# Kernel optimization log

Hardware: AMD Instinct MI355X
Metric: run time of the kernel (lower is better)

The kernel has to match this reference:

```python
import jax, jax.numpy as jnp
import numpy as np

BN_EPS = 1e-5


def _conv1x1(x, w, b=None):
    # x: [B,C,H,W], w: [O,C] (1x1 conv kernel squeezed)
    y = jnp.einsum('bchw,oc->bohw', x, w)
    if b is not None:
        y = y + b[None, :, None, None]
    return y


def _maxpool2(x):
    B, C, H, W = x.shape
    return x.reshape(B, C, H // 2, 2, W // 2, 2).max(axis=(3, 5))


def setup_inputs() -> dict:
    key = jax.random.key(0)
    ks = jax.random.split(key, 14)
    B, C, H, W = 8, 128, 64, 64
    IC = C // 2  # inter_channels
    s = 0.05
    f32 = jnp.float32
    return {
        'x': jax.random.normal(ks[0], (B, C, H, W), f32),
        'w1': jax.random.normal(ks[1], (IC, C), f32) * s,
        'b1': jax.random.normal(ks[2], (IC,), f32) * s,
        'w3': jax.random.normal(ks[3], (IC, C), f32) * s,
        'b3': jax.random.normal(ks[4], (IC,), f32) * s,
        'w4': jax.random.normal(ks[5], (IC, C), f32) * s,
        'b4': jax.random.normal(ks[6], (IC,), f32) * s,
        'w5': jax.random.normal(ks[7], (2 * IC,), f32) * s,  # conv5_pr, no bias
        'w2': jax.random.normal(ks[8], (C, IC), f32) * s,  # zero-init in torch; randomized for a non-trivial baseline
        'b2': jax.random.normal(ks[9], (C,), f32) * s,
        'bn_gamma': 1.0 + jax.random.normal(ks[10], (C,), f32) * 0.1,
        'bn_beta': jax.random.normal(ks[11], (C,), f32) * 0.1,
        'bn_mean': jax.random.normal(ks[12], (C,), f32) * 0.1,
        'bn_var': jax.random.uniform(ks[13], (C,), f32, 0.5, 1.5),
    }


def reference(x, w1, b1, w3, b3, w4, b4, w5, w2, b2, bn_gamma, bn_beta, bn_mean, bn_var):
    B, C, H, W = x.shape
    IC = C // 2
    N = H * W            # query positions
    # value branch: conv1 -> maxpool -> [B, M, IC]
    xg = _maxpool2(_conv1x1(x, w1, b1)).reshape(B, IC, -1)  # [B, IC, M]
    M = xg.shape[-1]
    xg = xg.transpose(0, 2, 1)  # [B, M, IC]
    # affinity: relu(w5 . cat(xt_i, xp_j)) is separable -> avoid [B,2IC,N,M] blowup
    xt = _conv1x1(x, w3, b3).reshape(B, IC, N)              # [B, IC, N]
    xp = _maxpool2(_conv1x1(x, w4, b4)).reshape(B, IC, M)   # [B, IC, M]
    wt, wp = w5[:IC], w5[IC:]
    logits = jnp.einsum('c,bcn->bn', wt, xt)[:, :, None] + \
             jnp.einsum('c,bcm->bm', wp, xp)[:, None, :]    # [B, N, M]
    feats = jax.nn.relu(logits) / M
    # aggregate
    y = jnp.einsum('bnm,bmi->bni', feats, xg)               # [B, N, IC]
    y = y.transpose(0, 2, 1).reshape(B, IC, H, W)
    # conv2 + batchnorm (eval mode, running stats)
    y = _conv1x1(y, w2, b2)
    inv = jax.lax.rsqrt(bn_var + BN_EPS)
    y = (y - bn_mean[None, :, None, None]) * (bn_gamma * inv)[None, :, None, None] + bn_beta[None, :, None, None]
    return y + x
```

## Files before the change

kernel.cpp:

```cpp
#include <hip/hip_runtime.h>

typedef unsigned int u32;
typedef unsigned short u16;

#define Cn 128
#define ICn 64
#define Nn 4096
#define Mn 1024

typedef __attribute__((ext_vector_type(8))) short s8v;
typedef __attribute__((ext_vector_type(4))) float f4v;

union U8 { uint4 u; s8v v; };

__device__ __forceinline__ float asf(u32 u){ union{u32 i; float f;} v; v.i = u; return v.f; }
__device__ __forceinline__ float bf2f(u16 u){ return asf(((u32)u) << 16); }
__device__ __forceinline__ u32 pk2(float lo, float hi){
    u32 r;
    asm("v_cvt_pk_bf16_f32 %0, %1, %2" : "=v"(r) : "v"(lo), "v"(hi));
    return r;
}
__device__ __forceinline__ u16 f2bf(float f){ return (u16)pk2(f, f); }

__global__ __launch_bounds__(256) void k_conv(
    const float* __restrict__ x,
    const float* __restrict__ w1, const float* __restrict__ b1,
    const float* __restrict__ w3, const float* __restrict__ b3,
    const float* __restrict__ w4, const float* __restrict__ b4,
    const float* __restrict__ w5,
    float* __restrict__ t_o, float* __restrict__ p_o, u16* __restrict__ xg_o)
{
    const int tile = blockIdx.x;
    const int r  = tile >> 1;
    const int wb = tile & 1;
    const int b  = blockIdx.y;
    const int tid = threadIdx.x;

    __shared__ __align__(16) u16 smem[35080];
    u16* xsT = smem;
    u16* w1t = smem + 8704;
    u16* w4t = smem + 17408;
    float* u3s = (float*)&smem[26112];
    float* ph0 = (float*)&smem[26372];
    float* ph1 = (float*)&smem[30724];

    #pragma unroll
    for (int it = 0; it < 4; ++it) {
        int f = tid + 256 * it;
        int cp = f >> 4, rem = f & 15;
        int rl = rem >> 3, wq = rem & 7;
        const float* src = x + ((size_t)(b * Cn + 2 * cp)) * Nn + (2 * r + rl) * 64 + 32 * wb + 4 * wq;
        float4 v0 = *(const float4*)src;
        float4 v1 = *(const float4*)(src + Nn);
        int lp0 = rl * 32 + 4 * wq;
        int cS = (2 * cp) ^ (wq << 3);
        *(u32*)&xsT[(lp0 + 0) * 136 + cS] = pk2(v0.x, v1.x);
        *(u32*)&xsT[(lp0 + 1) * 136 + cS] = pk2(v0.y, v1.y);
        *(u32*)&xsT[(lp0 + 2) * 136 + cS] = pk2(v0.z, v1.z);
        *(u32*)&xsT[(lp0 + 3) * 136 + cS] = pk2(v0.w, v1.w);
    }
    #pragma unroll
    for (int it = 0; it < 4; ++it) {
        int f = tid + 256 * it;
        int ic = f >> 4, cq = f & 15;
        const float4* s1 = (const float4*)&w1[f * 8];
        const float4* s4 = (const float4*)&w4[f * 8];
        float4 a0 = s1[0], a1v = s1[1];
        float4 d0 = s4[0], d1v = s4[1];
        uint4 A, D;
        A.x = pk2(a0.x, a0.y); A.y = pk2(a0.z, a0.w); A.z = pk2(a1v.x, a1v.y); A.w = pk2(a1v.z, a1v.w);
        D.x = pk2(d0.x, d0.y); D.y = pk2(d0.z, d0.w); D.z = pk2(d1v.x, d1v.y); D.w = pk2(d1v.z, d1v.w);
        *(uint4*)&w1t[ic * 136 + 8 * cq] = A;
        *(uint4*)&w4t[ic * 136 + 8 * cq] = D;
    }
    if (tid < 128) {
        float s0 = 0.f, s1 = 0.f;
        #pragma unroll 8
        for (int ic = 0; ic < 64; ic += 2) {
            s0 += w5[ic]     * w3[ic * Cn + tid];
            s1 += w5[ic + 1] * w3[(ic + 1) * Cn + tid];
        }
        u3s[tid] = s0 + s1;
    } else if (tid == 128) {
        float s = 0.f;
        #pragma unroll 16
        for (int ic = 0; ic < 64; ++ic) s += w5[ic] * b3[ic];
        u3s[128] = s;
    }
    __syncthreads();

    const int lane = tid & 63;
    const int wv   = tid >> 6;
    const int col  = lane & 15;
    const int quad = lane >> 4;

    f4v acc1[4] = {}, acc4[4] = {};
    const u16* xrow = &xsT[(16 * wv + col) * 136];
    const int xsw = (((16 * wv + col) >> 2) & 7) << 3;
    #pragma unroll
    for (int kb = 0; kb < 4; ++kb) {
        s8v bx = *(const s8v*)&xrow[(kb * 32 + quad * 8) ^ xsw];
        #pragma unroll
        for (int icb = 0; icb < 4; ++icb) {
            s8v a1 = *(const s8v*)&w1t[(icb * 16 + col) * 136 + kb * 32 + quad * 8];
            s8v a4 = *(const s8v*)&w4t[(icb * 16 + col) * 136 + kb * 32 + quad * 8];
            acc1[icb] = __builtin_amdgcn_mfma_f32_16x16x32_bf16(a1, bx, acc1[icb], 0, 0, 0);
            acc4[icb] = __builtin_amdgcn_mfma_f32_16x16x32_bf16(a4, bx, acc4[icb], 0, 0, 0);
        }
    }

    const int lp = 16 * wv + col;
    const int rl = lp >> 5, wl = lp & 31, pw = wl >> 1;
    const bool wr = (wl & 1) == 0;
    #pragma unroll
    for (int icb = 0; icb < 4; ++icb)
        #pragma unroll
        for (int reg = 0; reg < 4; ++reg) {
            float v1 = acc1[icb][reg];
            float m1 = fmaxf(v1, __shfl_xor(v1, 1, 64));
            float v4 = acc4[icb][reg];
            float m4 = fmaxf(v4, __shfl_xor(v4, 1, 64));
            if (wr) {
                ph0[(rl * 16 + pw) * 68 + icb * 16 + quad * 4 + reg] = m1;
                ph1[(rl * 16 + pw) * 68 + icb * 16 + quad * 4 + reg] = m4;
            }
        }
    __syncthreads();

    #pragma unroll
    for (int it = 0; it < 4; ++it) {
        int e = tid + 256 * it;
        int pwq = e >> 6, ic = e & 63;
        float v = fmaxf(ph0[pwq * 68 + ic], ph0[(16 + pwq) * 68 + ic]) + b1[ic];
        xg_o[((size_t)(b * 64 + ic) << 10) + r * 32 + wb * 16 + pwq] = f2bf(v * (1.0f / 1024.0f));
    }
    {
        int px = tid >> 2, part = tid & 3;
        const int tsw = ((px >> 2) & 7) << 3;
        const u16* xr = &xsT[px * 136];
        float s = 0.f;
        #pragma unroll
        for (int cq = 0; cq < 4; ++cq) {
            int u = part * 32 + cq * 8;
            s8v xv = *(const s8v*)&xr[u ^ tsw];
            #pragma unroll
            for (int j = 0; j < 8; ++j) s += u3s[u + j] * bf2f((u16)xv[j]);
        }
        s += __shfl_xor(s, 1, 64);
        s += __shfl_xor(s, 2, 64);
        if (part == 0)
            t_o[(size_t)b * Nn + (2 * r + (px >> 5)) * 64 + 32 * wb + (px & 31)] = s + u3s[128];
    }
    if (tid < 16) {
        float s = 0.f;
        #pragma unroll 8
        for (int ic = 0; ic < 64; ++ic) {
            float pv = fmaxf(ph1[tid * 68 + ic], ph1[(16 + tid) * 68 + ic]) + b4[ic];
            s += w5[64 + ic] * pv;
        }
        p_o[(size_t)b * Mn + r * 32 + wb * 16 + tid] = s;
    }
}

__global__ __launch_bounds__(512) void k_back(
    const float* __restrict__ x, const float* __restrict__ t,
    const float* __restrict__ p, const u16* __restrict__ xg,
    const float* __restrict__ w2, const float* __restrict__ b2,
    const float* __restrict__ gamma, const float* __restrict__ beta,
    const float* __restrict__ mean, const float* __restrict__ var,
    float* __restrict__ out)
{
    const int nt = blockIdx.x;
    const int b  = blockIdx.y;
    const int tid = threadIdx.x;

    __shared__ __align__(16) char smem[87808];
    u16* xgs  = (u16*)smem;
    u16* w2t  = (u16*)(smem + 32768);
    u32* ylds = (u32*)(smem + 49152);
    float* pl = (float*)(smem + 82176);
    float* tl = (float*)(smem + 86272);
    float* sc0 = (float*)(smem + 86784);
    float* sc1 = (float*)(smem + 87296);
    float* ytr = (float*)smem;

    pl[tid]       = p[b * Mn + tid];
    pl[tid + 512] = p[b * Mn + tid + 512];
    if (tid < 128) {
        tl[tid] = t[(size_t)b * Nn + nt * 128 + tid];
    } else if (tid < 256) {
        int co = tid - 128;
        float s = gamma[co] * rsqrtf(var[co] + 1e-5f);
        sc0[co] = s;
        sc1[co] = (b2[co] - mean[co]) * s + beta[co];
    }
    #pragma unroll
    for (int it = 0; it < 2; ++it) {
        int f = tid + 512 * it;
        int co = f >> 3, iq = f & 7;
        const float4* s2 = (const float4*)&w2[co * 64 + iq * 8];
        float4 a0 = s2[0], a1v = s2[1];
        uint4 V;
        V.x = pk2(a0.x, a0.y); V.y = pk2(a0.z, a0.w); V.z = pk2(a1v.x, a1v.y); V.w = pk2(a1v.z, a1v.w);
        *(uint4*)&w2t[co * 64 + ((iq * 8) ^ ((co & 7) << 3))] = V;
    }
    #pragma unroll
    for (int it = 0; it < 2; ++it) {
        int f = tid + 512 * it;
        int ic = f >> 4, mc = f & 15;
        uint4 V = *(const uint4*)&xg[((size_t)(b * 64 + ic) << 10) + mc * 8];
        *(uint4*)&xgs[ic * 128 + ((mc * 8) ^ ((ic & 7) << 3))] = V;
    }
    __syncthreads();

    const int lane = tid & 63;
    const int wv   = tid >> 6;
    const int col  = lane & 15;
    const int quad = lane >> 4;
    const int nb   = wv * 16;
    const int xsw  = (col & 7) << 3;
    const float tval = tl[nb + col];

    f4v acc[4] = {};
    for (int mt = 0; mt < 8; ++mt) {
        uint4 pf0, pf1;
        if (mt < 7) {
            int f0 = tid, f1 = tid + 512;
            pf0 = *(const uint4*)&xg[((size_t)(b * 64 + (f0 >> 4)) << 10) + (mt + 1) * 128 + (f0 & 15) * 8];
            pf1 = *(const uint4*)&xg[((size_t)(b * 64 + (f1 >> 4)) << 10) + (mt + 1) * 128 + (f1 & 15) * 8];
        }
        const u16* xb = xgs + (mt & 1) * 8192;
        #pragma unroll
        for (int kb = 0; kb < 4; ++kb) {
            int mb = mt * 128 + kb * 32;
            float4 pa = *(const float4*)&pl[mb + quad * 8];
            float4 pb = *(const float4*)&pl[mb + quad * 8 + 4];
            float f0 = fmaxf(tval + pa.x, 0.f), f1 = fmaxf(tval + pa.y, 0.f);
            float f2 = fmaxf(tval + pa.z, 0.f), f3 = fmaxf(tval + pa.w, 0.f);
            float f4 = fmaxf(tval + pb.x, 0.f), f5 = fmaxf(tval + pb.y, 0.f);
            float f6 = fmaxf(tval + pb.z, 0.f), f7 = fmaxf(tval + pb.w, 0.f);
            U8 hi, lo;
            hi.u.x = pk2(f0, f1); hi.u.y = pk2(f2, f3); hi.u.z = pk2(f4, f5); hi.u.w = pk2(f6, f7);
            float l0 = f0 - asf(hi.u.x << 16), l1 = f1 - asf(hi.u.x & 0xffff0000u);
            float l2 = f2 - asf(hi.u.y << 16), l3 = f3 - asf(hi.u.y & 0xffff0000u);
            float l4 = f4 - asf(hi.u.z << 16), l5 = f5 - asf(hi.u.z & 0xffff0000u);
            float l6 = f6 - asf(hi.u.w << 16), l7 = f7 - asf(hi.u.w & 0xffff0000u);
            lo.u.x = pk2(l0, l1); lo.u.y = pk2(l2, l3); lo.u.z = pk2(l4, l5); lo.u.w = pk2(l6, l7);
            #pragma unroll
            for (int icb = 0; icb < 4; ++icb) {
                const s8v bf = *(const s8v*)&xb[(icb * 16 + col) * 128 + ((kb * 32 + quad * 8) ^ xsw)];
                acc[icb] = __builtin_amdgcn_mfma_f32_16x16x32_bf16(hi.v, bf, acc[icb], 0, 0, 0);
                acc[icb] = __builtin_amdgcn_mfma_f32_16x16x32_bf16(lo.v, bf, acc[icb], 0, 0, 0);
            }
        }
        if (mt < 7) {
            int f0 = tid, f1 = tid + 512;
            u16* dst = xgs + ((mt + 1) & 1) * 8192;
            *(uint4*)&dst[(f0 >> 4) * 128 + (((f0 & 15) * 8) ^ (((f0 >> 4) & 7) << 3))] = pf0;
            *(uint4*)&dst[(f1 >> 4) * 128 + (((f1 & 15) * 8) ^ (((f1 >> 4) & 7) << 3))] = pf1;
        }
        __syncthreads();
    }

    #pragma unroll
    for (int icb = 0; icb < 4; ++icb)
        #pragma unroll
        for (int reg = 0; reg < 4; ++reg) {
            float f = acc[icb][reg];
            u32 h = pk2(f, f) & 0xffffu;
            float lo = f - asf(h << 16);
            u32 l = pk2(lo, lo) & 0xffffu;
            ylds[(icb * 16 + col) * 129 + nb + quad * 4 + reg] = h | (l << 16);
        }
    __syncthreads();

    f4v acc2[8] = {};
    #pragma unroll
    for (int kb = 0; kb < 2; ++kb) {
        u32 yv[8];
        #pragma unroll
        for (int j = 0; j < 8; ++j)
            yv[j] = ylds[(kb * 32 + quad * 8 + j) * 129 + nb + col];
        U8 bhi, blo;
        bhi.u.x = (yv[0] & 0xffffu) | (yv[1] << 16);
        bhi.u.y = (yv[2] & 0xffffu) | (yv[3] << 16);
        bhi.u.z = (yv[4] & 0xffffu) | (yv[5] << 16);
        bhi.u.w = (yv[6] & 0xffffu) | (yv[7] << 16);
        blo.u.x = (yv[0] >> 16) | (yv[1] & 0xffff0000u);
        blo.u.y = (yv[2] >> 16) | (yv[3] & 0xffff0000u);
        blo.u.z = (yv[4] >> 16) | (yv[5] & 0xffff0000u);
        blo.u.w = (yv[6] >> 16) | (yv[7] & 0xffff0000u);
        #pragma unroll
        for (int cob = 0; cob < 8; ++cob) {
            const s8v a = *(const s8v*)&w2t[(cob * 16 + col) * 64 + ((kb * 32 + quad * 8) ^ xsw)];
            acc2[cob] = __builtin_amdgcn_mfma_f32_16x16x32_bf16(a, bhi.v, acc2[cob], 0, 0, 0);
            acc2[cob] = __builtin_amdgcn_mfma_f32_16x16x32_bf16(a, blo.v, acc2[cob], 0, 0, 0);
        }
    }
    __syncthreads();

    #pragma unroll
    for (int cob = 0; cob < 8; ++cob)
        #pragma unroll
        for (int reg = 0; reg < 4; ++reg)
            ytr[(cob * 16 + quad * 4 + reg) * 132 + nb + col] = acc2[cob][reg];
    __syncthreads();

    const int n0g = nt * 128;
    #pragma unroll
    for (int it = 0; it < 8; ++it) {
        int f = tid + 512 * it;
        int co = f >> 5, nq = (f & 31) * 4;
        size_t gi = ((size_t)(b * Cn + co)) * Nn + n0g + nq;
        float4 xv = *(const float4*)&x[gi];
        float4 yv = *(const float4*)&ytr[co * 132 + nq];
        float s = sc0[co], bsv = sc1[co];
        float4 o;
        o.x = yv.x * s + bsv + xv.x;
        o.y = yv.y * s + bsv + xv.y;
        o.z = yv.z * s + bsv + xv.z;
        o.w = yv.w * s + bsv + xv.w;
        *(float4*)&out[gi] = o;
    }
}

extern "C" void kernel_launch(void* const* d_in, const int* in_sizes, int n_in,
                              void* d_out, int out_size, void* d_ws, size_t ws_size,
                              hipStream_t stream)
{
    const float* x  = (const float*)d_in[0];
    const float* w1 = (const float*)d_in[1];
    const float* b1 = (const float*)d_in[2];
    const float* w3 = (const float*)d_in[3];
    const float* b3 = (const float*)d_in[4];
    const float* w4 = (const float*)d_in[5];
    const float* b4 = (const float*)d_in[6];
    const float* w5 = (const float*)d_in[7];
    const float* w2 = (const float*)d_in[8];
    const float* b2 = (const float*)d_in[9];
    const float* gm = (const float*)d_in[10];
    const float* bt = (const float*)d_in[11];
    const float* mn = (const float*)d_in[12];
    const float* vr = (const float*)d_in[13];
    float* out = (float*)d_out;

    float* ws = (float*)d_ws;
    const size_t FTOT = 3823872;
    if (ws_size < FTOT * sizeof(float)) return;

    float* t_w  = ws;
    float* p_w  = ws + 32768;
    u16*   xg_w = (u16*)(ws + 40960);

    k_conv<<<dim3(64, 8), 256, 0, stream>>>(x, w1, b1, w3, b3, w4, b4, w5,
                                            t_w, p_w, xg_w);
    k_back<<<dim3(32, 8), 512, 0, stream>>>(x, t_w, p_w, xg_w,
                                            w2, b2, gm, bt, mn, vr, out);
}
```

Measured before the change: 119.4 us.

## Halve k_back tile to 64 queries and parallelize p reduction across threads

```diff
diff --git a/kernel.cpp b/kernel.cpp
--- a/kernel.cpp
+++ b/kernel.cpp
@@ -151,18 +151,25 @@
         if (part == 0)
             t_o[(size_t)b * Nn + (2 * r + (px >> 5)) * 64 + 32 * wb + (px & 31)] = s + u3s[128];
     }
-    if (tid < 16) {
+    {
+        int pwq = tid >> 4, j16 = tid & 15;
         float s = 0.f;
-        #pragma unroll 8
-        for (int ic = 0; ic < 64; ++ic) {
-            float pv = fmaxf(ph1[tid * 68 + ic], ph1[(16 + tid) * 68 + ic]) + b4[ic];
+        #pragma unroll
+        for (int jj = 0; jj < 4; ++jj) {
+            int ic = j16 + 16 * jj;
+            float pv = fmaxf(ph1[pwq * 68 + ic], ph1[(16 + pwq) * 68 + ic]) + b4[ic];
             s += w5[64 + ic] * pv;
         }
-        p_o[(size_t)b * Mn + r * 32 + wb * 16 + tid] = s;
+        s += __shfl_xor(s, 1, 64);
+        s += __shfl_xor(s, 2, 64);
+        s += __shfl_xor(s, 4, 64);
+        s += __shfl_xor(s, 8, 64);
+        if (j16 == 0)
+            p_o[(size_t)b * Mn + r * 32 + wb * 16 + pwq] = s;
     }
 }
 
-__global__ __launch_bounds__(512) void k_back(
+__global__ __launch_bounds__(256) void k_back(
     const float* __restrict__ x, const float* __restrict__ t,
     const float* __restrict__ p, const u16* __restrict__ xg,
     const float* __restrict__ w2, const float* __restrict__ b2,
@@ -174,29 +181,29 @@
     const int b  = blockIdx.y;
     const int tid = threadIdx.x;
 
-    __shared__ __align__(16) char smem[87808];
+    __shared__ __align__(16) char smem[71936];
     u16* xgs  = (u16*)smem;
     u16* w2t  = (u16*)(smem + 32768);
     u32* ylds = (u32*)(smem + 49152);
-    float* pl = (float*)(smem + 82176);
-    float* tl = (float*)(smem + 86272);
-    float* sc0 = (float*)(smem + 86784);
-    float* sc1 = (float*)(smem + 87296);
+    float* pl = (float*)(smem + 66560);
+    float* tl = (float*)(smem + 70656);
+    float* sc0 = (float*)(smem + 70912);
+    float* sc1 = (float*)(smem + 71424);
     float* ytr = (float*)smem;
 
-    pl[tid]       = p[b * Mn + tid];
-    pl[tid + 512] = p[b * Mn + tid + 512];
-    if (tid < 128) {
-        tl[tid] = t[(size_t)b * Nn + nt * 128 + tid];
-    } else if (tid < 256) {
+    #pragma unroll
+    for (int it = 0; it < 4; ++it) pl[tid + 256 * it] = p[b * Mn + tid + 256 * it];
+    if (tid < 64) {
+        tl[tid] = t[(size_t)b * Nn + nt * 64 + tid];
+    } else if (tid >= 128) {
         int co = tid - 128;
         float s = gamma[co] * rsqrtf(var[co] + 1e-5f);
         sc0[co] = s;
         sc1[co] = (b2[co] - mean[co]) * s + beta[co];
     }
     #pragma unroll
-    for (int it = 0; it < 2; ++it) {
-        int f = tid + 512 * it;
+    for (int it = 0; it < 4; ++it) {
+        int f = tid + 256 * it;
         int co = f >> 3, iq = f & 7;
         const float4* s2 = (const float4*)&w2[co * 64 + iq * 8];
         float4 a0 = s2[0], a1v = s2[1];
@@ -205,8 +212,8 @@
         *(uint4*)&w2t[co * 64 + ((iq * 8) ^ ((co & 7) << 3))] = V;
     }
     #pragma unroll
-    for (int it = 0; it < 2; ++it) {
-        int f = tid + 512 * it;
+    for (int it = 0; it < 4; ++it) {
+        int f = tid + 256 * it;
         int ic = f >> 4, mc = f & 15;
         uint4 V = *(const uint4*)&xg[((size_t)(b * 64 + ic) << 10) + mc * 8];
         *(uint4*)&xgs[ic * 128 + ((mc * 8) ^ ((ic & 7) << 3))] = V;
@@ -223,11 +230,13 @@
 
     f4v acc[4] = {};
     for (int mt = 0; mt < 8; ++mt) {
-        uint4 pf0, pf1;
+        uint4 pf[4];
         if (mt < 7) {
-            int f0 = tid, f1 = tid + 512;
-            pf0 = *(const uint4*)&xg[((size_t)(b * 64 + (f0 >> 4)) << 10) + (mt + 1) * 128 + (f0 & 15) * 8];
-            pf1 = *(const uint4*)&xg[((size_t)(b * 64 + (f1 >> 4)) << 10) + (mt + 1) * 128 + (f1 & 15) * 8];
+            #pragma unroll
+            for (int j = 0; j < 4; ++j) {
+                int f = tid + 256 * j;
+                pf[j] = *(const uint4*)&xg[((size_t)(b * 64 + (f >> 4)) << 10) + (mt + 1) * 128 + (f & 15) * 8];
+            }
         }
         const u16* xb = xgs + (mt & 1) * 8192;
         #pragma unroll
@@ -254,10 +263,12 @@
             }
         }
         if (mt < 7) {
-            int f0 = tid, f1 = tid + 512;
             u16* dst = xgs + ((mt + 1) & 1) * 8192;
-            *(uint4*)&dst[(f0 >> 4) * 128 + (((f0 & 15) * 8) ^ (((f0 >> 4) & 7) << 3))] = pf0;
-            *(uint4*)&dst[(f1 >> 4) * 128 + (((f1 & 15) * 8) ^ (((f1 >> 4) & 7) << 3))] = pf1;
+            #pragma unroll
+            for (int j = 0; j < 4; ++j) {
+                int f = tid + 256 * j;
+                *(uint4*)&dst[(f >> 4) * 128 + (((f & 15) * 8) ^ (((f >> 4) & 7) << 3))] = pf[j];
+            }
         }
         __syncthreads();
     }
@@ -270,7 +281,7 @@
             u32 h = pk2(f, f) & 0xffffu;
             float lo = f - asf(h << 16);
             u32 l = pk2(lo, lo) & 0xffffu;
-            ylds[(icb * 16 + col) * 129 + nb + quad * 4 + reg] = h | (l << 16);
+            ylds[(icb * 16 + col) * 68 + nb + quad * 4 + reg] = h | (l << 16);
         }
     __syncthreads();
 
@@ -280,7 +291,7 @@
         u32 yv[8];
         #pragma unroll
         for (int j = 0; j < 8; ++j)
-            yv[j] = ylds[(kb * 32 + quad * 8 + j) * 129 + nb + col];
+            yv[j] = ylds[(kb * 32 + quad * 8 + j) * 68 + nb + col];
         U8 bhi, blo;
         bhi.u.x = (yv[0] & 0xffffu) | (yv[1] << 16);
         bhi.u.y = (yv[2] & 0xffffu) | (yv[3] << 16);
@@ -303,17 +314,17 @@
     for (int cob = 0; cob < 8; ++cob)
         #pragma unroll
         for (int reg = 0; reg < 4; ++reg)
-            ytr[(cob * 16 + quad * 4 + reg) * 132 + nb + col] = acc2[cob][reg];
-    __syncthreads();
-
-    const int n0g = nt * 128;
+            ytr[(cob * 16 + quad * 4 + reg) * 68 + nb + col] = acc2[cob][reg];
+    __syncthreads();
+
+    const int n0g = nt * 64;
     #pragma unroll
     for (int it = 0; it < 8; ++it) {
-        int f = tid + 512 * it;
-        int co = f >> 5, nq = (f & 31) * 4;
+        int f = tid + 256 * it;
+        int co = f >> 4, nq = (f & 15) * 4;
         size_t gi = ((size_t)(b * Cn + co)) * Nn + n0g + nq;
         float4 xv = *(const float4*)&x[gi];
-        float4 yv = *(const float4*)&ytr[co * 132 + nq];
+        float4 yv = *(const float4*)&ytr[co * 68 + nq];
         float s = sc0[co], bsv = sc1[co];
         float4 o;
         o.x = yv.x * s + bsv + xv.x;
@@ -354,6 +365,6 @@
 
     k_conv<<<dim3(64, 8), 256, 0, stream>>>(x, w1, b1, w3, b3, w4, b4, w5,
                                             t_w, p_w, xg_w);
-    k_back<<<dim3(32, 8), 512, 0, stream>>>(x, t_w, p_w, xg_w,
+    k_back<<<dim3(64, 8), 256, 0, stream>>>(x, t_w, p_w, xg_w,
                                             w2, b2, gm, bt, mn, vr, out);
 }
```

Measured after the change: 116.3 us. 1.03x faster.
